# Kernel tuning notes

Measured on AMD Instinct MI355X. Metric: run time of the kernel, lower is better.

Reference implementation:

```python
import jax, jax.numpy as jnp
import numpy as np

B, S, H = 2, 2048, 1024
NH, HD = 16, 64  # num_heads, head_dim
NEG = -1e9


def setup_inputs() -> dict:
    key = jax.random.key(0)
    ks = jax.random.split(key, 5)
    hidden_states = jax.random.normal(ks[0], (B, S, H), dtype=jnp.float32)
    # additive causal mask, broadcast over batch and heads
    causal = jnp.tril(jnp.ones((S, S), dtype=bool))
    attention_mask = jnp.where(causal, 0.0, NEG).astype(jnp.float32)[None, None]
    W_attn = jax.random.normal(ks[1], (H, 3 * H), dtype=jnp.float32) * 0.02
    b_attn = jax.random.normal(ks[2], (3 * H,), dtype=jnp.float32) * 0.02
    W_proj = jax.random.normal(ks[3], (H, H), dtype=jnp.float32) * 0.02
    b_proj = jax.random.normal(ks[4], (H,), dtype=jnp.float32) * 0.02
    return {"hidden_states": hidden_states, "attention_mask": attention_mask,
            "W_attn": W_attn, "b_attn": b_attn, "W_proj": W_proj, "b_proj": b_proj}


def reference(hidden_states, attention_mask, W_attn, b_attn, W_proj, b_proj):
    scale = HD ** -0.5
    # fused QKV projection: [B,S,3H]
    qkv = hidden_states @ W_attn + b_attn
    q, k, v = jnp.split(qkv, 3, axis=-1)
    # [B,S,H] -> [B,NH,S,HD]
    def heads(x):
        return x.reshape(B, S, NH, HD).transpose(0, 2, 1, 3)
    q, k, v = heads(q), heads(k), heads(v)
    # vanilla (prefill) attention: scores [B,NH,S,S]
    scores = jnp.einsum('bhqd,bhkd->bhqk', q, k) * scale + attention_mask
    probs = jax.nn.softmax(scores, axis=-1)
    ctx = jnp.einsum('bhqk,bhkd->bhqd', probs, v)
    # merge heads and output projection
    out = ctx.transpose(0, 2, 1, 3).reshape(B, S, H)
    return out @ W_proj + b_proj
```

## Files before the change

### kernel.cpp

```cpp
#include <hip/hip_runtime.h>
#include <hip/hip_bf16.h>

#define B_  2
#define S_  2048
#define H_  1024
#define NH_ 16
#define HD_ 64

typedef __attribute__((ext_vector_type(8))) short bf16x8;
typedef __attribute__((ext_vector_type(4))) float f32x4;
typedef __attribute__((ext_vector_type(4))) int   i32x4;

static __device__ __forceinline__ unsigned short f2bf(float f) {
    union { float f; unsigned int u; } v; v.f = f;
    unsigned int r = v.u + 0x7FFFu + ((v.u >> 16) & 1u);
    return (unsigned short)(r >> 16);
}
static __device__ __forceinline__ unsigned cvtpk(float a, float b) {
    unsigned r;
    asm("v_cvt_pk_bf16_f32 %0, %1, %2" : "=v"(r) : "v"(a), "v"(b));
    return r;
}

static __device__ __forceinline__ void barrier_keep_vmem() {
    __builtin_amdgcn_sched_barrier(0);
    asm volatile("s_waitcnt lgkmcnt(0)" ::: "memory");
    __builtin_amdgcn_s_barrier();
    __builtin_amdgcn_sched_barrier(0);
}
static __device__ __forceinline__ void barrier_exec_only() {
    __builtin_amdgcn_sched_barrier(0);
    __builtin_amdgcn_s_barrier();
    __builtin_amdgcn_sched_barrier(0);
}

__global__ __launch_bounds__(256) void to_bf16_kernel(
    const float* __restrict__ x, unsigned short* __restrict__ y, int n4)
{
    int i = blockIdx.x * 256 + threadIdx.x;
    if (i < n4) {
        float4 v = ((const float4*)x)[i];
        ushort4 o;
        o.x = f2bf(v.x); o.y = f2bf(v.y); o.z = f2bf(v.z); o.w = f2bf(v.w);
        ((ushort4*)y)[i] = o;
    }
}

__global__ __launch_bounds__(256) void transpose_to_bf16(
    const float* __restrict__ W, unsigned short* __restrict__ Wt, int K, int N)
{
    __shared__ unsigned short t[64][65];
    const int n0 = blockIdx.x * 64, k0 = blockIdx.y * 64;
    const int tid = threadIdx.x;
    #pragma unroll
    for (int i = 0; i < 16; ++i) {
        int idx = tid + i * 256; int r = idx >> 6, c = idx & 63;
        t[c][r] = f2bf(W[(size_t)(k0 + r) * N + n0 + c]);
    }
    __syncthreads();
    #pragma unroll
    for (int i = 0; i < 16; ++i) {
        int idx = tid + i * 256; int r = idx >> 6, c = idx & 63;
        Wt[(size_t)(n0 + r) * K + k0 + c] = t[r][c];
    }
}

template<int OUT_BF16>
__global__ __launch_bounds__(256) void gemm_mfma(
    const unsigned short* __restrict__ A,
    const unsigned short* __restrict__ Bt,
    const float* __restrict__ bias, void* __restrict__ Cv,
    int M, int N, int K)
{
    __shared__ __align__(16) unsigned short As[128][40];
    __shared__ __align__(16) unsigned short Bs[128][40];
    const int tid = threadIdx.x;
    const int lane = tid & 63, wave = tid >> 6;
    const int lr = lane & 15, lk = lane >> 4;
    const int wr = (wave >> 1) * 64, wc = (wave & 1) * 64;
    const int bm = blockIdx.y * 128, bn = blockIdx.x * 128;

    const int r0 = tid >> 2, r1 = r0 + 64;
    const int cc = (tid & 3) * 8;

    const unsigned short* pa0 = A  + (size_t)(bm + r0) * K + cc;
    const unsigned short* pa1 = A  + (size_t)(bm + r1) * K + cc;
    const unsigned short* pb0 = Bt + (size_t)(bn + r0) * K + cc;
    const unsigned short* pb1 = Bt + (size_t)(bn + r1) * K + cc;

    i32x4 ra0 = *(const i32x4*)pa0;
    i32x4 ra1 = *(const i32x4*)pa1;
    i32x4 rb0 = *(const i32x4*)pb0;
    i32x4 rb1 = *(const i32x4*)pb1;

    f32x4 acc[4][4];
    #pragma unroll
    for (int i = 0; i < 4; ++i)
        #pragma unroll
        for (int j = 0; j < 4; ++j)
            acc[i][j] = (f32x4){0.f, 0.f, 0.f, 0.f};

    for (int k0 = 0; k0 < K; k0 += 32) {
        *(i32x4*)&As[r0][cc] = ra0;
        *(i32x4*)&As[r1][cc] = ra1;
        *(i32x4*)&Bs[r0][cc] = rb0;
        *(i32x4*)&Bs[r1][cc] = rb1;
        barrier_keep_vmem();
        if (k0 + 32 < K) {
            ra0 = *(const i32x4*)(pa0 + k0 + 32);
            ra1 = *(const i32x4*)(pa1 + k0 + 32);
            rb0 = *(const i32x4*)(pb0 + k0 + 32);
            rb1 = *(const i32x4*)(pb1 + k0 + 32);
        }
        bf16x8 af[4], bfr[4];
        #pragma unroll
        for (int mi = 0; mi < 4; ++mi)
            af[mi] = *(const bf16x8*)&As[wr + mi * 16 + lr][lk * 8];
        #pragma unroll
        for (int ni = 0; ni < 4; ++ni)
            bfr[ni] = *(const bf16x8*)&Bs[wc + ni * 16 + lr][lk * 8];
        __builtin_amdgcn_s_setprio(1);
        #pragma unroll
        for (int mi = 0; mi < 4; ++mi)
            #pragma unroll
            for (int ni = 0; ni < 4; ++ni)
                acc[mi][ni] = __builtin_amdgcn_mfma_f32_16x16x32_bf16(
                    af[mi], bfr[ni], acc[mi][ni], 0, 0, 0);
        __builtin_amdgcn_s_setprio(0);
        barrier_exec_only();
    }

    #pragma unroll
    for (int ni = 0; ni < 4; ++ni) {
        const int col = bn + wc + ni * 16 + lr;
        const float bb = bias[col];
        #pragma unroll
        for (int mi = 0; mi < 4; ++mi) {
            #pragma unroll
            for (int r = 0; r < 4; ++r) {
                const int row = bm + wr + mi * 16 + lk * 4 + r;
                float v = acc[mi][ni][r] + bb;
                if (OUT_BF16)
                    ((unsigned short*)Cv)[(size_t)row * N + col] = f2bf(v);
                else
                    ((float*)Cv)[(size_t)row * N + col] = v;
            }
        }
    }
}

__global__ __launch_bounds__(256) void attn_mfma(
    const unsigned short* __restrict__ qkv, unsigned short* __restrict__ ctx)
{
    __shared__ __align__(16) unsigned short Ks[2][64][76];
    __shared__ __align__(16) unsigned short Vt[2][64][76];

    const int id   = blockIdx.x + 16 * (blockIdx.y + 16 * blockIdx.z);
    const int xcd  = id & 7, slot = id >> 3;
    const int pair = slot >> 2;
    const int hb   = xcd + 8 * (slot & 3);
    const int h = hb & 15, b = hb >> 4;

    const int tid = threadIdx.x, wave = tid >> 6, lane = tid & 63;
    const int lr = lane & 15, lk = lane >> 4;

    const int sr  = tid >> 3;
    const int scc = (tid & 7) * 8;
    const int rot = tid & 7;

    const float SC2  = 0.125f * 1.44269504089f;
    const float NM2C = -8.0f * 1.44269504089f;

    int buf = 0;
    #pragma unroll 1
    for (int half = 0; half < 2; ++half) {
        const int qt = half ? pair : (31 - pair);
        const int q0 = qt * 64;
        const int qW = q0 + wave * 16;
        const int qRow = qW + lr;
        const int nkt = qt + 1;

        const size_t qbase = (size_t)(b * S_ + qW + lr) * 3072 + h * 64;
        const bf16x8 qf0 = *(const bf16x8*)(qkv + qbase + lk * 8);
        const bf16x8 qf1 = *(const bf16x8*)(qkv + qbase + 32 + lk * 8);

        f32x4 oacc[4];
        #pragma unroll
        for (int d = 0; d < 4; ++d) oacc[d] = (f32x4){0.f, 0.f, 0.f, 0.f};
        float lpart = 0.0f;

        const size_t sbase = (size_t)(b * S_ + sr) * 3072 + h * 64 + scc;
        i32x4 kreg0 = *(const i32x4*)(qkv + sbase + 1024);
        i32x4 kreg1 = *(const i32x4*)(qkv + sbase + (size_t)32 * 3072 + 1024);
        i32x4 vreg0 = *(const i32x4*)(qkv + sbase + 2048);
        i32x4 vreg1 = *(const i32x4*)(qkv + sbase + (size_t)32 * 3072 + 2048);

        for (int kt = 0; kt < nkt; ++kt) {
            const int k0 = kt * 64;
            *(i32x4*)&Ks[buf][sr][scc]      = kreg0;
            *(i32x4*)&Ks[buf][sr + 32][scc] = kreg1;
            {
                const unsigned short* v0 = (const unsigned short*)&vreg0;
                const unsigned short* v1 = (const unsigned short*)&vreg1;
                #pragma unroll
                for (int jj = 0; jj < 8; ++jj) {
                    const int j = (jj + rot) & 7;
                    Vt[buf][scc + j][sr]      = v0[j];
                    Vt[buf][scc + j][sr + 32] = v1[j];
                }
            }
            barrier_keep_vmem();
            if (kt + 1 < nkt) {
                const size_t nb = sbase + (size_t)(k0 + 64) * 3072;
                kreg0 = *(const i32x4*)(qkv + nb + 1024);
                kreg1 = *(const i32x4*)(qkv + nb + (size_t)32 * 3072 + 1024);
                vreg0 = *(const i32x4*)(qkv + nb + 2048);
                vreg1 = *(const i32x4*)(qkv + nb + (size_t)32 * 3072 + 2048);
            }

            if (k0 <= qW + 15) {
                f32x4 st[4];
                #pragma unroll
                for (int kb = 0; kb < 4; ++kb) st[kb] = (f32x4){0.f, 0.f, 0.f, 0.f};
                __builtin_amdgcn_s_setprio(1);
                #pragma unroll
                for (int kb = 0; kb < 4; ++kb) {
                    bf16x8 k0f = *(const bf16x8*)&Ks[buf][kb * 16 + lr][lk * 8];
                    bf16x8 k1f = *(const bf16x8*)&Ks[buf][kb * 16 + lr][32 + lk * 8];
                    st[kb] = __builtin_amdgcn_mfma_f32_16x16x32_bf16(k0f, qf0, st[kb], 0, 0, 0);
                    st[kb] = __builtin_amdgcn_mfma_f32_16x16x32_bf16(k1f, qf1, st[kb], 0, 0, 0);
                }
                __builtin_amdgcn_s_setprio(0);

                if (k0 + 63 > qW) {
                    #pragma unroll
                    for (int kb = 0; kb < 4; ++kb)
                        #pragma unroll
                        for (int r = 0; r < 4; ++r)
                            if (k0 + kb * 16 + lk * 4 + r > qRow) st[kb][r] = -3.0e38f;
                }

                unsigned pw[8];
                float psum = 0.0f;
                #pragma unroll
                for (int kb = 0; kb < 4; ++kb) {
                    float e0 = __builtin_amdgcn_exp2f(fmaf(st[kb][0], SC2, NM2C));
                    float e1 = __builtin_amdgcn_exp2f(fmaf(st[kb][1], SC2, NM2C));
                    float e2 = __builtin_amdgcn_exp2f(fmaf(st[kb][2], SC2, NM2C));
                    float e3 = __builtin_amdgcn_exp2f(fmaf(st[kb][3], SC2, NM2C));
                    psum += (e0 + e1) + (e2 + e3);
                    pw[kb * 2 + 0] = cvtpk(e0, e1);
                    pw[kb * 2 + 1] = cvtpk(e2, e3);
                }
                lpart += psum;

                const i32x4 pa0i = {(int)pw[0], (int)pw[1], (int)pw[2], (int)pw[3]};
                const i32x4 pa1i = {(int)pw[4], (int)pw[5], (int)pw[6], (int)pw[7]};
                const bf16x8 pa0 = __builtin_bit_cast(bf16x8, pa0i);
                const bf16x8 pa1 = __builtin_bit_cast(bf16x8, pa1i);

                __builtin_amdgcn_s_setprio(1);
                #pragma unroll
                for (int d = 0; d < 4; ++d) {
                    const int dc = d * 16 + lr;
                    uint2 lo0 = *(const uint2*)&Vt[buf][dc][4 * lk];
                    uint2 hi0 = *(const uint2*)&Vt[buf][dc][16 + 4 * lk];
                    uint2 lo1 = *(const uint2*)&Vt[buf][dc][32 + 4 * lk];
                    uint2 hi1 = *(const uint2*)&Vt[buf][dc][48 + 4 * lk];
                    const i32x4 v0i = {(int)lo0.x, (int)lo0.y, (int)hi0.x, (int)hi0.y};
                    const i32x4 v1i = {(int)lo1.x, (int)lo1.y, (int)hi1.x, (int)hi1.y};
                    const bf16x8 vb0 = __builtin_bit_cast(bf16x8, v0i);
                    const bf16x8 vb1 = __builtin_bit_cast(bf16x8, v1i);
                    oacc[d] = __builtin_amdgcn_mfma_f32_16x16x32_bf16(pa0, vb0, oacc[d], 0, 0, 0);
                    oacc[d] = __builtin_amdgcn_mfma_f32_16x16x32_bf16(pa1, vb1, oacc[d], 0, 0, 0);
                }
                __builtin_amdgcn_s_setprio(0);
            }
            buf ^= 1;
        }

        float l = lpart;
        l += __shfl_xor(l, 16);
        l += __shfl_xor(l, 32);
        const float linv = 1.0f / l;
        float iv[4];
        #pragma unroll
        for (int r = 0; r < 4; ++r)
            iv[r] = __shfl(linv, (lane & 48) | ((lane >> 2) & 12) | r);
        #pragma unroll
        for (int r = 0; r < 4; ++r) {
            const size_t orow = (size_t)(b * S_ + qW + lk * 4 + r) * 1024 + h * 64;
            #pragma unroll
            for (int d = 0; d < 4; ++d)
                ctx[orow + d * 16 + lr] = f2bf(oacc[d][r] * iv[r]);
        }
    }
}

extern "C" void kernel_launch(void* const* d_in, const int* in_sizes, int n_in,
                              void* d_out, int out_size, void* d_ws, size_t ws_size,
                              hipStream_t stream)
{
    const float* hidden = (const float*)d_in[0];
    const float* W_attn = (const float*)d_in[2];
    const float* b_attn = (const float*)d_in[3];
    const float* W_proj = (const float*)d_in[4];
    const float* b_proj = (const float*)d_in[5];
    float* out = (float*)d_out;

    unsigned short* hid_bf  = (unsigned short*)d_ws;
    unsigned short* wattn_t = hid_bf  + (size_t)4096 * 1024;
    unsigned short* wproj_t = wattn_t + (size_t)3072 * 1024;
    unsigned short* qkv     = wproj_t + (size_t)1024 * 1024;
    unsigned short* ctx     = qkv     + (size_t)4096 * 3072;

    to_bf16_kernel<<<4096, 256, 0, stream>>>(hidden, hid_bf, 4096 * 1024 / 4);
    transpose_to_bf16<<<dim3(3072 / 64, 1024 / 64), 256, 0, stream>>>(
        W_attn, wattn_t, 1024, 3072);
    transpose_to_bf16<<<dim3(1024 / 64, 1024 / 64), 256, 0, stream>>>(
        W_proj, wproj_t, 1024, 1024);

    gemm_mfma<1><<<dim3(3072 / 128, 4096 / 128), 256, 0, stream>>>(
        hid_bf, wattn_t, b_attn, qkv, 4096, 3072, 1024);

    attn_mfma<<<dim3(16, NH_, B_), 256, 0, stream>>>(qkv, ctx);

    gemm_mfma<0><<<dim3(1024 / 128, 4096 / 128), 256, 0, stream>>>(
        ctx, wproj_t, b_proj, out, 4096, 1024, 1024);
}
```

Baseline: 142.5 us.

## Load GEMM tiles directly global-to-LDS and drop register prefetch

The GEMM mainloop now uses global_load_lds to move A and B tiles straight into shared memory, replacing the path that loaded into registers and then stored to LDS. To fit that instruction's layout, the LDS tiles lose their 40-element padding and become unpadded 32-wide rows. The register double-buffer prefetch is gone, so each iteration loads and then waits at a full __syncthreads before computing, with nothing overlapping the load. The unpadded layout may also cause LDS bank conflicts on the fragment reads.

```diff
diff --git a/kernel.cpp b/kernel.cpp
--- a/kernel.cpp
+++ b/kernel.cpp
@@ -22,14 +22,15 @@
     return r;
 }
 
+static __device__ __forceinline__ void gload_lds16(const void* g, void* l) {
+    __builtin_amdgcn_global_load_lds(
+        (const __attribute__((address_space(1))) void*)g,
+        (__attribute__((address_space(3))) void*)l, 16, 0, 0);
+}
+
 static __device__ __forceinline__ void barrier_keep_vmem() {
     __builtin_amdgcn_sched_barrier(0);
     asm volatile("s_waitcnt lgkmcnt(0)" ::: "memory");
-    __builtin_amdgcn_s_barrier();
-    __builtin_amdgcn_sched_barrier(0);
-}
-static __device__ __forceinline__ void barrier_exec_only() {
-    __builtin_amdgcn_sched_barrier(0);
     __builtin_amdgcn_s_barrier();
     __builtin_amdgcn_sched_barrier(0);
 }
@@ -72,26 +73,27 @@
     const float* __restrict__ bias, void* __restrict__ Cv,
     int M, int N, int K)
 {
-    __shared__ __align__(16) unsigned short As[128][40];
-    __shared__ __align__(16) unsigned short Bs[128][40];
+    __shared__ __align__(16) unsigned short As[128][32];
+    __shared__ __align__(16) unsigned short Bs[128][32];
     const int tid = threadIdx.x;
     const int lane = tid & 63, wave = tid >> 6;
     const int lr = lane & 15, lk = lane >> 4;
     const int wr = (wave >> 1) * 64, wc = (wave & 1) * 64;
     const int bm = blockIdx.y * 128, bn = blockIdx.x * 128;
 
-    const int r0 = tid >> 2, r1 = r0 + 64;
-    const int cc = (tid & 3) * 8;
-
-    const unsigned short* pa0 = A  + (size_t)(bm + r0) * K + cc;
-    const unsigned short* pa1 = A  + (size_t)(bm + r1) * K + cc;
-    const unsigned short* pb0 = Bt + (size_t)(bn + r0) * K + cc;
-    const unsigned short* pb1 = Bt + (size_t)(bn + r1) * K + cc;
-
-    i32x4 ra0 = *(const i32x4*)pa0;
-    i32x4 ra1 = *(const i32x4*)pa1;
-    i32x4 rb0 = *(const i32x4*)pb0;
-    i32x4 rb1 = *(const i32x4*)pb1;
+    const int u0 = wave * 2, u1 = wave * 2 + 1;
+    const int gr0 = u0 * 16 + (lane >> 2);
+    const int gr1 = u1 * 16 + (lane >> 2);
+    const int gc  = (lane & 3) * 8;
+
+    const unsigned short* pag0 = A  + (size_t)(bm + gr0) * K + gc;
+    const unsigned short* pag1 = A  + (size_t)(bm + gr1) * K + gc;
+    const unsigned short* pbg0 = Bt + (size_t)(bn + gr0) * K + gc;
+    const unsigned short* pbg1 = Bt + (size_t)(bn + gr1) * K + gc;
+    unsigned short* la0 = &As[u0 * 16][0];
+    unsigned short* la1 = &As[u1 * 16][0];
+    unsigned short* lb0 = &Bs[u0 * 16][0];
+    unsigned short* lb1 = &Bs[u1 * 16][0];
 
     f32x4 acc[4][4];
     #pragma unroll
@@ -101,17 +103,12 @@
             acc[i][j] = (f32x4){0.f, 0.f, 0.f, 0.f};
 
     for (int k0 = 0; k0 < K; k0 += 32) {
-        *(i32x4*)&As[r0][cc] = ra0;
-        *(i32x4*)&As[r1][cc] = ra1;
-        *(i32x4*)&Bs[r0][cc] = rb0;
-        *(i32x4*)&Bs[r1][cc] = rb1;
-        barrier_keep_vmem();
-        if (k0 + 32 < K) {
-            ra0 = *(const i32x4*)(pa0 + k0 + 32);
-            ra1 = *(const i32x4*)(pa1 + k0 + 32);
-            rb0 = *(const i32x4*)(pb0 + k0 + 32);
-            rb1 = *(const i32x4*)(pb1 + k0 + 32);
-        }
+        gload_lds16(pag0 + k0, la0);
+        gload_lds16(pag1 + k0, la1);
+        gload_lds16(pbg0 + k0, lb0);
+        gload_lds16(pbg1 + k0, lb1);
+        __syncthreads();
+
         bf16x8 af[4], bfr[4];
         #pragma unroll
         for (int mi = 0; mi < 4; ++mi)
@@ -127,7 +124,7 @@
                 acc[mi][ni] = __builtin_amdgcn_mfma_f32_16x16x32_bf16(
                     af[mi], bfr[ni], acc[mi][ni], 0, 0, 0);
         __builtin_amdgcn_s_setprio(0);
-        barrier_exec_only();
+        __syncthreads();
     }
 
     #pragma unroll
```

Result: slower. 148.7 us (+4.3%).

## Enlarge attention query tile to 128 rows with 512-thread blocks

Applied to the files above, without the earlier changes.

The attention kernel now runs 8 waves per block, each block covering 128 query rows instead of 64, so every K/V tile staged in shared memory serves twice as many queries. The grid halves to 256 blocks, the block-to-XCD mapping is simplified, and the causal pair balancing now works on 16 query tiles. Each thread loads one K/V row chunk instead of two, and the custom barrier is replaced by __syncthreads. The aim is to cut repeated global K/V loads. The cost is fewer blocks for occupancy and a possibly heavier barrier that may not keep outstanding vector-memory loads in flight.

```diff
diff --git a/kernel.cpp b/kernel.cpp
--- a/kernel.cpp
+++ b/kernel.cpp
@@ -149,16 +149,15 @@
     }
 }
 
-__global__ __launch_bounds__(256) void attn_mfma(
+__global__ __launch_bounds__(512) void attn_mfma(
     const unsigned short* __restrict__ qkv, unsigned short* __restrict__ ctx)
 {
     __shared__ __align__(16) unsigned short Ks[2][64][76];
     __shared__ __align__(16) unsigned short Vt[2][64][76];
 
-    const int id   = blockIdx.x + 16 * (blockIdx.y + 16 * blockIdx.z);
-    const int xcd  = id & 7, slot = id >> 3;
-    const int pair = slot >> 2;
-    const int hb   = xcd + 8 * (slot & 3);
+    const int id   = blockIdx.x + 8 * (blockIdx.y + 16 * blockIdx.z);
+    const int hb   = (id & 7) + 8 * ((id >> 3) & 3);
+    const int pair = id >> 5;
     const int h = hb & 15, b = hb >> 4;
 
     const int tid = threadIdx.x, wave = tid >> 6, lane = tid & 63;
@@ -174,11 +173,11 @@
     int buf = 0;
     #pragma unroll 1
     for (int half = 0; half < 2; ++half) {
-        const int qt = half ? pair : (31 - pair);
-        const int q0 = qt * 64;
+        const int qt = half ? pair : (15 - pair);
+        const int q0 = qt * 128;
         const int qW = q0 + wave * 16;
         const int qRow = qW + lr;
-        const int nkt = qt + 1;
+        const int nkt = 2 * qt + 2;
 
         const size_t qbase = (size_t)(b * S_ + qW + lr) * 3072 + h * 64;
         const bf16x8 qf0 = *(const bf16x8*)(qkv + qbase + lk * 8);
@@ -190,32 +189,25 @@
         float lpart = 0.0f;
 
         const size_t sbase = (size_t)(b * S_ + sr) * 3072 + h * 64 + scc;
-        i32x4 kreg0 = *(const i32x4*)(qkv + sbase + 1024);
-        i32x4 kreg1 = *(const i32x4*)(qkv + sbase + (size_t)32 * 3072 + 1024);
-        i32x4 vreg0 = *(const i32x4*)(qkv + sbase + 2048);
-        i32x4 vreg1 = *(const i32x4*)(qkv + sbase + (size_t)32 * 3072 + 2048);
+        i32x4 kreg = *(const i32x4*)(qkv + sbase + 1024);
+        i32x4 vreg = *(const i32x4*)(qkv + sbase + 2048);
 
         for (int kt = 0; kt < nkt; ++kt) {
             const int k0 = kt * 64;
-            *(i32x4*)&Ks[buf][sr][scc]      = kreg0;
-            *(i32x4*)&Ks[buf][sr + 32][scc] = kreg1;
+            *(i32x4*)&Ks[buf][sr][scc] = kreg;
             {
-                const unsigned short* v0 = (const unsigned short*)&vreg0;
-                const unsigned short* v1 = (const unsigned short*)&vreg1;
+                const unsigned short* vp = (const unsigned short*)&vreg;
                 #pragma unroll
                 for (int jj = 0; jj < 8; ++jj) {
                     const int j = (jj + rot) & 7;
-                    Vt[buf][scc + j][sr]      = v0[j];
-                    Vt[buf][scc + j][sr + 32] = v1[j];
+                    Vt[buf][scc + j][sr] = vp[j];
                 }
             }
-            barrier_keep_vmem();
+            __syncthreads();
             if (kt + 1 < nkt) {
                 const size_t nb = sbase + (size_t)(k0 + 64) * 3072;
-                kreg0 = *(const i32x4*)(qkv + nb + 1024);
-                kreg1 = *(const i32x4*)(qkv + nb + (size_t)32 * 3072 + 1024);
-                vreg0 = *(const i32x4*)(qkv + nb + 2048);
-                vreg1 = *(const i32x4*)(qkv + nb + (size_t)32 * 3072 + 2048);
+                kreg = *(const i32x4*)(qkv + nb + 1024);
+                vreg = *(const i32x4*)(qkv + nb + 2048);
             }
 
             if (k0 <= qW + 15) {
@@ -323,7 +315,7 @@
     gemm_mfma<1><<<dim3(3072 / 128, 4096 / 128), 256, 0, stream>>>(
         hid_bf, wattn_t, b_attn, qkv, 4096, 3072, 1024);
 
-    attn_mfma<<<dim3(16, NH_, B_), 256, 0, stream>>>(qkv, ctx);
+    attn_mfma<<<dim3(8, NH_, B_), 512, 0, stream>>>(qkv, ctx);
 
     gemm_mfma<0><<<dim3(1024 / 128, 4096 / 128), 256, 0, stream>>>(
         ctx, wproj_t, b_proj, out, 4096, 1024, 1024);
```

New measurement: 129.1 us. 9.5% less time.
